# Kernel tuning notes

Hardware: AMD Instinct MI355X
Metric: run time of the kernel (lower is better)

Reference implementation:

```python
import jax, jax.numpy as jnp
import numpy as np

N, C, T = 64, 512, 64
P = N * (N - 1) // 2  # 2016 pairs


def _maxpool2x2(h):
    p, c, H, W = h.shape
    return h.reshape(p, c, H // 2, 2, W // 2, 2).max(axis=(3, 5))


def setup_inputs() -> dict:
    key = jax.random.key(0)
    ks = jax.random.split(key, 16)
    s = lambda k, shape, fan: jax.random.normal(k, shape, jnp.float32) * (1.0 / np.sqrt(fan))
    return {
        "x": jax.random.normal(ks[0], (N, C, T), jnp.float32),
        "w_conv1d": s(ks[1], (256, 512), 512),  # Conv1d(512,256,k=1) weight squeezed
        "b_conv1d": jnp.zeros((256,), jnp.float32),
        "w_c1": s(ks[2], (32, 512), 512),       # Conv2d(512,32,1x1)
        "b_c1": jnp.zeros((32,), jnp.float32),
        "w_c2": s(ks[3], (8, 32), 32),          # Conv2d(32,8,1x1)
        "b_c2": jnp.zeros((8,), jnp.float32),
        "w_fc1": s(ks[4], (32, 64), 64),
        "b_fc1": jnp.zeros((32,), jnp.float32),
        "w_fc2": s(ks[5], (8, 32), 32),
        "b_fc2": jnp.zeros((8,), jnp.float32),
        "w_fc3": s(ks[6], (1, 8), 8),
        "b_fc3": jnp.zeros((1,), jnp.float32),
        "w_mlp": s(ks[7], (1, C * T), C * T),   # stand-in my_fc: Linear(512*T,1)
        "b_mlp": jnp.zeros((1,), jnp.float32),
    }


def reference(x, w_conv1d, b_conv1d, w_c1, b_c1, w_c2, b_c2,
              w_fc1, b_fc1, w_fc2, b_fc2, w_fc3, b_fc3, w_mlp, b_mlp):
    # per-sample score head (my_fc stand-in)
    score = jax.nn.sigmoid(x.reshape(N, -1) @ w_mlp.T + b_mlp)  # [N,1]
    # shared conv1d over all samples at once (original does it per-pair)
    f = jnp.einsum("nct,oc->not", x, w_conv1d) + b_conv1d[None, :, None]  # [N,256,T]
    ii, jj = jnp.triu_indices(N, k=1)  # P pairs, same order as the nested loop
    # pairwise correlation matrix: einsum('abd,acd->abc')
    M = jnp.einsum("pct,pdt->pcd", f[ii], f[jj])  # [P,256,256]
    M = M.reshape(P, 512, 32, 4)
    h = jnp.einsum("pchw,oc->pohw", M, w_c1) + b_c1[None, :, None, None]
    h = _maxpool2x2(h)  # [P,32,16,2]
    h = jnp.einsum("pchw,oc->pohw", h, w_c2) + b_c2[None, :, None, None]
    h = _maxpool2x2(h)  # [P,8,8,1]
    v = h.reshape(P, 64)
    v = jax.nn.relu(v @ w_fc1.T + b_fc1)
    v = jax.nn.relu(v @ w_fc2.T + b_fc2)
    group_score = jax.nn.sigmoid(v @ w_fc3.T + b_fc3).reshape(-1)  # [P]
    return score, group_score
```

## Files before the change

### kernel.cpp

```cpp
#include <hip/hip_runtime.h>
#include <hip/hip_bf16.h>
#include <math.h>


typedef __attribute__((ext_vector_type(8))) short short8;
typedef __attribute__((ext_vector_type(4))) float f32x4;

__device__ __forceinline__ unsigned short f2bf(float f) {
    __hip_bfloat16 h = __float2bfloat16(f);
    return *reinterpret_cast<unsigned short*>(&h);
}

__global__ __launch_bounds__(256) void k_wa_part(
    const float* __restrict__ w_c1, const float* __restrict__ w_conv,
    float* __restrict__ Wpart)
{
    int b = blockIdx.x, q = blockIdx.y;
    int r = b >> 1;
    int cin = (b & 1) * 256 + threadIdx.x;
    int s = r >> 5, o = r & 31;
    const float* wrow = w_c1 + o * 512 + s;
    const float* wcp  = w_conv + cin;
    float acc = 0.f;
    #pragma unroll 8
    for (int c = q * 64; c < q * 64 + 64; ++c)
        acc += wrow[2 * c] * wcp[c * 512];
    Wpart[(q * 64 + r) * 512 + cin] = acc;
}

__global__ __launch_bounds__(256) void k_wprep(
    const float* __restrict__ w_conv1d, const float* __restrict__ Wpart,
    const float* __restrict__ b_conv1d, const float* __restrict__ w_c1,
    unsigned short* __restrict__ Wb, float* __restrict__ Gb)
{
    int idx = blockIdx.x * 256 + threadIdx.x;
    int m = idx >> 7, c4 = (idx & 127) * 4;
    float4 v;
    if (m < 256) {
        v = *reinterpret_cast<const float4*>(w_conv1d + m * 512 + c4);
    } else {
        const float* p0 = Wpart + (m - 256) * 512 + c4;
        float4 a = *reinterpret_cast<const float4*>(p0);
        float4 b = *reinterpret_cast<const float4*>(p0 + 32768);
        float4 c = *reinterpret_cast<const float4*>(p0 + 65536);
        float4 d = *reinterpret_cast<const float4*>(p0 + 98304);
        v.x = a.x + b.x + c.x + d.x;
        v.y = a.y + b.y + c.y + d.y;
        v.z = a.z + b.z + c.z + d.z;
        v.w = a.w + b.w + c.w + d.w;
    }
    ushort4 u;
    u.x = f2bf(v.x); u.y = f2bf(v.y); u.z = f2bf(v.z); u.w = f2bf(v.w);
    *reinterpret_cast<ushort4*>(Wb + m * 512 + c4) = u;

    if (blockIdx.x == 0) {
        __shared__ float abred[256];
        Gb[threadIdx.x] = b_conv1d[threadIdx.x];
        int r = threadIdx.x & 63, q = threadIdx.x >> 6;
        int s = r >> 5, o = r & 31;
        const float* wr2 = w_c1 + o * 512 + s;
        float a = 0.f;
        #pragma unroll 8
        for (int c = q * 64; c < q * 64 + 64; ++c)
            a += wr2[2 * c] * b_conv1d[c];
        abred[threadIdx.x] = a;
        __syncthreads();
        if (threadIdx.x < 64)
            Gb[256 + threadIdx.x] = abred[threadIdx.x] + abred[threadIdx.x + 64]
                                  + abred[threadIdx.x + 128] + abred[threadIdx.x + 192];
    }
}

__global__ __launch_bounds__(256) void k_xprep(
    const float* __restrict__ x, unsigned short* __restrict__ xxT)
{
    __shared__ float tile[64][65];
    int n = blockIdx.x, c0 = blockIdx.y * 64;
    int tid = threadIdx.x;
    int cl = tid >> 4, t4 = (tid & 15) * 4;
    const float* xp = x + n * 32768 + c0 * 64;
    #pragma unroll
    for (int p = 0; p < 4; ++p) {
        int c = cl + p * 16;
        float4 v = *reinterpret_cast<const float4*>(xp + c * 64 + t4);
        tile[t4 + 0][c] = v.x; tile[t4 + 1][c] = v.y;
        tile[t4 + 2][c] = v.z; tile[t4 + 3][c] = v.w;
    }
    __syncthreads();
    int tl = tid >> 4, cl4 = (tid & 15) * 4;
    #pragma unroll
    for (int p = 0; p < 4; ++p) {
        int t = tl + p * 16;
        ushort4 u;
        u.x = f2bf(tile[t][cl4 + 0]);
        u.y = f2bf(tile[t][cl4 + 1]);
        u.z = f2bf(tile[t][cl4 + 2]);
        u.w = f2bf(tile[t][cl4 + 3]);
        *reinterpret_cast<ushort4*>(xxT + n * 32768 + t * 512 + c0 + cl4) = u;
    }
}

__global__ __launch_bounds__(256) void k_fgemm(
    const unsigned short* __restrict__ Wb, const unsigned short* __restrict__ xxT,
    const float* __restrict__ Gb, unsigned short* __restrict__ FTTb,
    unsigned short* __restrict__ ALb)
{
    int n = blockIdx.x, mg = blockIdx.y, nt = blockIdx.z;
    int tid = threadIdx.x, l = tid & 63, w = tid >> 6;
    int m0 = mg * 64 + w * 16;
    int t0 = nt * 16;
    int r15 = l & 15, kg = l >> 4;
    const unsigned short* ap = Wb + (m0 + r15) * 512 + kg * 8;
    const unsigned short* bp = xxT + n * 32768 + (t0 + r15) * 512 + kg * 8;
    f32x4 acc = {0.f, 0.f, 0.f, 0.f};
    #pragma unroll
    for (int ks = 0; ks < 16; ++ks) {
        short8 a = *reinterpret_cast<const short8*>(ap + ks * 32);
        short8 b = *reinterpret_cast<const short8*>(bp + ks * 32);
        acc = __builtin_amdgcn_mfma_f32_16x16x32_bf16(a, b, acc, 0, 0, 0);
    }
    int t = t0 + r15;
    int mrow = m0 + kg * 4;
    float4 gb = *reinterpret_cast<const float4*>(Gb + mrow);
    float gbv[4] = {gb.x, gb.y, gb.z, gb.w};
    if (m0 < 256) {
        #pragma unroll
        for (int r = 0; r < 4; ++r) {
            int m = mrow + r;
            int e = m & 127, s = m >> 7, kp = s * 64 + t;
            int off = (((e << 8) + (kp << 1)) ^ ((e & 7) << 4)) >> 1;
            FTTb[n * 16384 + off] = f2bf(acc[r] + gbv[r]);
        }
    } else {
        #pragma unroll
        for (int r = 0; r < 4; ++r) {
            int m = mrow + r;
            int rr = m - 256, o = rr & 31, sA = rr >> 5, kp = sA * 64 + t;
            int off = (((o << 8) + (kp << 1)) ^ ((o & 7) << 4)) >> 1;
            ALb[n * 4096 + off] = f2bf(acc[r] + gbv[r]);
        }
    }
}

__global__ __launch_bounds__(256) void k_score_part(
    const float* __restrict__ x, const float* __restrict__ wm,
    float* __restrict__ part)
{
    int n = blockIdx.x, c4 = blockIdx.y;
    const float4* x4 = reinterpret_cast<const float4*>(x + n * 32768) + c4 * 2048;
    const float4* w4 = reinterpret_cast<const float4*>(wm) + c4 * 2048;
    float acc = 0.f;
    for (int u = threadIdx.x; u < 2048; u += 256) {
        float4 a = x4[u], w = w4[u];
        acc += a.x * w.x + a.y * w.y + a.z * w.z + a.w * w.w;
    }
    for (int off = 32; off; off >>= 1) acc += __shfl_down(acc, off, 64);
    __shared__ float red[4];
    if ((threadIdx.x & 63) == 0) red[threadIdx.x >> 6] = acc;
    __syncthreads();
    if (threadIdx.x == 0)
        part[n * 4 + c4] = red[0] + red[1] + red[2] + red[3];
}

__global__ __launch_bounds__(256) void k_pairs(
    const char* __restrict__ FTTb, const char* __restrict__ ALb,
    const float* __restrict__ b_c1, const float* __restrict__ w_c2,
    const float* __restrict__ b_c2, const float* __restrict__ w_fc1,
    const float* __restrict__ b_fc1, const float* __restrict__ w_fc2,
    const float* __restrict__ b_fc2, const float* __restrict__ w_fc3,
    const float* __restrict__ b_fc3, const float* __restrict__ part,
    const float* __restrict__ bm, float* __restrict__ out)
{
    __shared__ uint4 smq[2560];
    char* sm = (char*)smq;
    int p = blockIdx.x;
    int i = 0, rem = p;
    while (rem >= 63 - i) { rem -= 63 - i; ++i; }
    int j = i + 1 + rem;
    int tid = threadIdx.x;

    if (p == 0 && tid >= 128 && tid < 192) {
        int n = tid - 128;
        float s = part[n * 4] + part[n * 4 + 1] + part[n * 4 + 2]
                + part[n * 4 + 3] + bm[0];
        out[n] = 1.f / (1.f + expf(-s));
    }

    {
        const uint4* sA = reinterpret_cast<const uint4*>(ALb + (size_t)i * 8192);
        uint4* dA = reinterpret_cast<uint4*>(sm);
        #pragma unroll
        for (int u = 0; u < 2; ++u) dA[tid + 256 * u] = sA[tid + 256 * u];
        const uint4* sB = reinterpret_cast<const uint4*>(FTTb + (size_t)j * 32768);
        uint4* dB = reinterpret_cast<uint4*>(sm + 8192);
        #pragma unroll
        for (int u = 0; u < 8; ++u) dB[tid + 256 * u] = sB[tid + 256 * u];
    }
    __syncthreads();

    int l = tid & 63, wid = tid >> 6;
    int col = l & 15;
    int lk16 = (l >> 4) << 4;
    int xr = (col & 7) << 4;
    int oa0 = col, oa1 = col + 16;
    int e0 = wid * 32 + col, e1 = e0 + 16;

    f32x4 acc00 = {0.f,0.f,0.f,0.f}, acc01 = {0.f,0.f,0.f,0.f};
    f32x4 acc10 = {0.f,0.f,0.f,0.f}, acc11 = {0.f,0.f,0.f,0.f};
    #pragma unroll
    for (int ks = 0; ks < 4; ++ks) {
        int kb = ks * 64 + lk16;
        short8 a0 = *reinterpret_cast<const short8*>(sm + (((oa0 << 8) + kb) ^ xr));
        short8 a1 = *reinterpret_cast<const short8*>(sm + (((oa1 << 8) + kb) ^ xr));
        short8 b0 = *reinterpret_cast<const short8*>(sm + 8192 + (((e0 << 8) + kb) ^ xr));
        short8 b1 = *reinterpret_cast<const short8*>(sm + 8192 + (((e1 << 8) + kb) ^ xr));
        acc00 = __builtin_amdgcn_mfma_f32_16x16x32_bf16(a0, b0, acc00, 0, 0, 0);
        acc01 = __builtin_amdgcn_mfma_f32_16x16x32_bf16(a0, b1, acc01, 0, 0, 0);
        acc10 = __builtin_amdgcn_mfma_f32_16x16x32_bf16(a1, b0, acc10, 0, 0, 0);
        acc11 = __builtin_amdgcn_mfma_f32_16x16x32_bf16(a1, b1, acc11, 0, 0, 0);
    }
    __syncthreads();

    float* H = (float*)sm;
    int rowbase = (l >> 4) * 4;
    #pragma unroll
    for (int r4 = 0; r4 < 4; ++r4) {
        int o0 = rowbase + r4, o1 = o0 + 16;
        float bb0 = b_c1[o0], bb1 = b_c1[o1];
        H[o0 * 128 + e0] = acc00[r4] + bb0;
        H[o0 * 128 + e1] = acc01[r4] + bb0;
        H[o1 * 128 + e0] = acc10[r4] + bb1;
        H[o1 * 128 + e1] = acc11[r4] + bb1;
    }
    __syncthreads();

    float* PL = (float*)(sm + 16384);
    for (int idx = tid; idx < 1024; idx += 256) {
        int o = idx >> 5, h2 = (idx >> 1) & 15, w2 = idx & 1;
        const float* hp = H + o * 128 + h2 * 8 + w2 * 2;
        PL[o * 32 + h2 * 2 + w2] =
            fmaxf(fmaxf(hp[0], hp[1]), fmaxf(hp[4], hp[5]));
    }
    __syncthreads();

    float* C2 = (float*)(sm + 20480);
    {
        int o2 = tid >> 5, pos = tid & 31;
        float a2 = b_c2[o2];
        #pragma unroll 8
        for (int o = 0; o < 32; ++o) a2 += w_c2[o2 * 32 + o] * PL[o * 32 + pos];
        C2[o2 * 32 + pos] = a2;
    }
    __syncthreads();

    float* V = (float*)(sm + 21504);
    if (tid < 64) {
        int o2 = tid >> 3, h3 = tid & 7;
        const float* cp = C2 + o2 * 32 + h3 * 4;
        V[tid] = fmaxf(fmaxf(cp[0], cp[1]), fmaxf(cp[2], cp[3]));
    }
    __syncthreads();

    float* R1 = (float*)(sm + 21760);
    if (tid < 32) {
        float a = b_fc1[tid];
        const float* wr = w_fc1 + tid * 64;
        #pragma unroll 8
        for (int u = 0; u < 64; ++u) a += wr[u] * V[u];
        R1[tid] = fmaxf(a, 0.f);
    }
    __syncthreads();

    float* R2 = (float*)(sm + 21888);
    if (tid < 8) {
        float a = b_fc2[tid];
        #pragma unroll 8
        for (int u = 0; u < 32; ++u) a += w_fc2[tid * 32 + u] * R1[u];
        R2[tid] = fmaxf(a, 0.f);
    }
    __syncthreads();

    if (tid == 0) {
        float a = b_fc3[0];
        #pragma unroll
        for (int u = 0; u < 8; ++u) a += w_fc3[u] * R2[u];
        out[64 + p] = 1.f / (1.f + expf(-a));
    }
}

extern "C" void kernel_launch(void* const* d_in, const int* in_sizes, int n_in,
                              void* d_out, int out_size, void* d_ws, size_t ws_size,
                              hipStream_t stream) {
    const float* x        = (const float*)d_in[0];
    const float* w_conv1d = (const float*)d_in[1];
    const float* b_conv1d = (const float*)d_in[2];
    const float* w_c1     = (const float*)d_in[3];
    const float* b_c1     = (const float*)d_in[4];
    const float* w_c2     = (const float*)d_in[5];
    const float* b_c2     = (const float*)d_in[6];
    const float* w_fc1    = (const float*)d_in[7];
    const float* b_fc1    = (const float*)d_in[8];
    const float* w_fc2    = (const float*)d_in[9];
    const float* b_fc2    = (const float*)d_in[10];
    const float* w_fc3    = (const float*)d_in[11];
    const float* b_fc3    = (const float*)d_in[12];
    const float* w_mlp    = (const float*)d_in[13];
    const float* b_mlp    = (const float*)d_in[14];
    float* out = (float*)d_out;

    char* base = (char*)d_ws;
    unsigned short* xxT   = (unsigned short*)(base);
    unsigned short* FTTb  = (unsigned short*)(base + 4194304);
    unsigned short* ALb   = (unsigned short*)(base + 6291456);
    unsigned short* Wb    = (unsigned short*)(base + 6815744);
    float*          Wpart = (float*)(base + 7143424);
    float*          Gb    = (float*)(base + 7667712);
    float*          part  = (float*)(base + 7669760);

    hipLaunchKernelGGL(k_wa_part, dim3(128, 4), dim3(256), 0, stream,
                       w_c1, w_conv1d, Wpart);
    hipLaunchKernelGGL(k_wprep, dim3(160), dim3(256), 0, stream,
                       w_conv1d, Wpart, b_conv1d, w_c1, Wb, Gb);
    hipLaunchKernelGGL(k_xprep, dim3(64, 8), dim3(256), 0, stream, x, xxT);
    hipLaunchKernelGGL(k_score_part, dim3(64, 4), dim3(256), 0, stream,
                       x, w_mlp, part);
    hipLaunchKernelGGL(k_fgemm, dim3(64, 5, 4), dim3(256), 0, stream,
                       Wb, xxT, Gb, FTTb, ALb);
    hipLaunchKernelGGL(k_pairs, dim3(2016), dim3(256), 0, stream,
                       (const char*)FTTb, (const char*)ALb,
                       b_c1, w_c2, b_c2, w_fc1, b_fc1,
                       w_fc2, b_fc2, w_fc3, b_fc3, part, b_mlp, out);
}
```

Before: 141.3 us.

## Fuse all six kernels into one cooperative persistent kernel with grid syncs

Replaces the six separate launches with a single cooperative kernel of 512 persistent blocks. The stages are separated by grid-wide barriers, and each stage loops over its original work items. This removes the per-launch overhead and the gaps between kernels. In exchange it adds three grid.sync barriers, caps parallelism in the pairs stage at 512 resident blocks, and mixes the work item types of the first stage into one loop.

Measured after the change: 466.9 us. 230% more time.

```diff
diff --git a/kernel.cpp b/kernel.cpp
--- a/kernel.cpp
+++ b/kernel.cpp
@@ -1,6 +1,9 @@
 #include <hip/hip_runtime.h>
 #include <hip/hip_bf16.h>
+#include <hip/hip_cooperative_groups.h>
 #include <math.h>
+
+namespace cg = cooperative_groups;
 
 
 typedef __attribute__((ext_vector_type(8))) short short8;
@@ -11,280 +14,281 @@
     return *reinterpret_cast<unsigned short*>(&h);
 }
 
-__global__ __launch_bounds__(256) void k_wa_part(
-    const float* __restrict__ w_c1, const float* __restrict__ w_conv,
-    float* __restrict__ Wpart)
-{
-    int b = blockIdx.x, q = blockIdx.y;
-    int r = b >> 1;
-    int cin = (b & 1) * 256 + threadIdx.x;
-    int s = r >> 5, o = r & 31;
-    const float* wrow = w_c1 + o * 512 + s;
-    const float* wcp  = w_conv + cin;
-    float acc = 0.f;
-    #pragma unroll 8
-    for (int c = q * 64; c < q * 64 + 64; ++c)
-        acc += wrow[2 * c] * wcp[c * 512];
-    Wpart[(q * 64 + r) * 512 + cin] = acc;
-}
-
-__global__ __launch_bounds__(256) void k_wprep(
-    const float* __restrict__ w_conv1d, const float* __restrict__ Wpart,
+__global__ __launch_bounds__(256, 2) void k_mega(
+    const float* __restrict__ x, const float* __restrict__ w_conv1d,
     const float* __restrict__ b_conv1d, const float* __restrict__ w_c1,
-    unsigned short* __restrict__ Wb, float* __restrict__ Gb)
-{
-    int idx = blockIdx.x * 256 + threadIdx.x;
-    int m = idx >> 7, c4 = (idx & 127) * 4;
-    float4 v;
-    if (m < 256) {
-        v = *reinterpret_cast<const float4*>(w_conv1d + m * 512 + c4);
-    } else {
-        const float* p0 = Wpart + (m - 256) * 512 + c4;
-        float4 a = *reinterpret_cast<const float4*>(p0);
-        float4 b = *reinterpret_cast<const float4*>(p0 + 32768);
-        float4 c = *reinterpret_cast<const float4*>(p0 + 65536);
-        float4 d = *reinterpret_cast<const float4*>(p0 + 98304);
-        v.x = a.x + b.x + c.x + d.x;
-        v.y = a.y + b.y + c.y + d.y;
-        v.z = a.z + b.z + c.z + d.z;
-        v.w = a.w + b.w + c.w + d.w;
-    }
-    ushort4 u;
-    u.x = f2bf(v.x); u.y = f2bf(v.y); u.z = f2bf(v.z); u.w = f2bf(v.w);
-    *reinterpret_cast<ushort4*>(Wb + m * 512 + c4) = u;
-
-    if (blockIdx.x == 0) {
-        __shared__ float abred[256];
-        Gb[threadIdx.x] = b_conv1d[threadIdx.x];
-        int r = threadIdx.x & 63, q = threadIdx.x >> 6;
-        int s = r >> 5, o = r & 31;
-        const float* wr2 = w_c1 + o * 512 + s;
-        float a = 0.f;
-        #pragma unroll 8
-        for (int c = q * 64; c < q * 64 + 64; ++c)
-            a += wr2[2 * c] * b_conv1d[c];
-        abred[threadIdx.x] = a;
-        __syncthreads();
-        if (threadIdx.x < 64)
-            Gb[256 + threadIdx.x] = abred[threadIdx.x] + abred[threadIdx.x + 64]
-                                  + abred[threadIdx.x + 128] + abred[threadIdx.x + 192];
-    }
-}
-
-__global__ __launch_bounds__(256) void k_xprep(
-    const float* __restrict__ x, unsigned short* __restrict__ xxT)
-{
-    __shared__ float tile[64][65];
-    int n = blockIdx.x, c0 = blockIdx.y * 64;
-    int tid = threadIdx.x;
-    int cl = tid >> 4, t4 = (tid & 15) * 4;
-    const float* xp = x + n * 32768 + c0 * 64;
-    #pragma unroll
-    for (int p = 0; p < 4; ++p) {
-        int c = cl + p * 16;
-        float4 v = *reinterpret_cast<const float4*>(xp + c * 64 + t4);
-        tile[t4 + 0][c] = v.x; tile[t4 + 1][c] = v.y;
-        tile[t4 + 2][c] = v.z; tile[t4 + 3][c] = v.w;
-    }
-    __syncthreads();
-    int tl = tid >> 4, cl4 = (tid & 15) * 4;
-    #pragma unroll
-    for (int p = 0; p < 4; ++p) {
-        int t = tl + p * 16;
-        ushort4 u;
-        u.x = f2bf(tile[t][cl4 + 0]);
-        u.y = f2bf(tile[t][cl4 + 1]);
-        u.z = f2bf(tile[t][cl4 + 2]);
-        u.w = f2bf(tile[t][cl4 + 3]);
-        *reinterpret_cast<ushort4*>(xxT + n * 32768 + t * 512 + c0 + cl4) = u;
-    }
-}
-
-__global__ __launch_bounds__(256) void k_fgemm(
-    const unsigned short* __restrict__ Wb, const unsigned short* __restrict__ xxT,
-    const float* __restrict__ Gb, unsigned short* __restrict__ FTTb,
-    unsigned short* __restrict__ ALb)
-{
-    int n = blockIdx.x, mg = blockIdx.y, nt = blockIdx.z;
-    int tid = threadIdx.x, l = tid & 63, w = tid >> 6;
-    int m0 = mg * 64 + w * 16;
-    int t0 = nt * 16;
-    int r15 = l & 15, kg = l >> 4;
-    const unsigned short* ap = Wb + (m0 + r15) * 512 + kg * 8;
-    const unsigned short* bp = xxT + n * 32768 + (t0 + r15) * 512 + kg * 8;
-    f32x4 acc = {0.f, 0.f, 0.f, 0.f};
-    #pragma unroll
-    for (int ks = 0; ks < 16; ++ks) {
-        short8 a = *reinterpret_cast<const short8*>(ap + ks * 32);
-        short8 b = *reinterpret_cast<const short8*>(bp + ks * 32);
-        acc = __builtin_amdgcn_mfma_f32_16x16x32_bf16(a, b, acc, 0, 0, 0);
-    }
-    int t = t0 + r15;
-    int mrow = m0 + kg * 4;
-    float4 gb = *reinterpret_cast<const float4*>(Gb + mrow);
-    float gbv[4] = {gb.x, gb.y, gb.z, gb.w};
-    if (m0 < 256) {
-        #pragma unroll
-        for (int r = 0; r < 4; ++r) {
-            int m = mrow + r;
-            int e = m & 127, s = m >> 7, kp = s * 64 + t;
-            int off = (((e << 8) + (kp << 1)) ^ ((e & 7) << 4)) >> 1;
-            FTTb[n * 16384 + off] = f2bf(acc[r] + gbv[r]);
-        }
-    } else {
-        #pragma unroll
-        for (int r = 0; r < 4; ++r) {
-            int m = mrow + r;
-            int rr = m - 256, o = rr & 31, sA = rr >> 5, kp = sA * 64 + t;
-            int off = (((o << 8) + (kp << 1)) ^ ((o & 7) << 4)) >> 1;
-            ALb[n * 4096 + off] = f2bf(acc[r] + gbv[r]);
-        }
-    }
-}
-
-__global__ __launch_bounds__(256) void k_score_part(
-    const float* __restrict__ x, const float* __restrict__ wm,
-    float* __restrict__ part)
-{
-    int n = blockIdx.x, c4 = blockIdx.y;
-    const float4* x4 = reinterpret_cast<const float4*>(x + n * 32768) + c4 * 2048;
-    const float4* w4 = reinterpret_cast<const float4*>(wm) + c4 * 2048;
-    float acc = 0.f;
-    for (int u = threadIdx.x; u < 2048; u += 256) {
-        float4 a = x4[u], w = w4[u];
-        acc += a.x * w.x + a.y * w.y + a.z * w.z + a.w * w.w;
-    }
-    for (int off = 32; off; off >>= 1) acc += __shfl_down(acc, off, 64);
-    __shared__ float red[4];
-    if ((threadIdx.x & 63) == 0) red[threadIdx.x >> 6] = acc;
-    __syncthreads();
-    if (threadIdx.x == 0)
-        part[n * 4 + c4] = red[0] + red[1] + red[2] + red[3];
-}
-
-__global__ __launch_bounds__(256) void k_pairs(
-    const char* __restrict__ FTTb, const char* __restrict__ ALb,
     const float* __restrict__ b_c1, const float* __restrict__ w_c2,
     const float* __restrict__ b_c2, const float* __restrict__ w_fc1,
     const float* __restrict__ b_fc1, const float* __restrict__ w_fc2,
     const float* __restrict__ b_fc2, const float* __restrict__ w_fc3,
-    const float* __restrict__ b_fc3, const float* __restrict__ part,
-    const float* __restrict__ bm, float* __restrict__ out)
+    const float* __restrict__ b_fc3, const float* __restrict__ w_mlp,
+    const float* __restrict__ b_mlp,
+    unsigned short* __restrict__ xxT, unsigned short* __restrict__ FTTb,
+    unsigned short* __restrict__ ALb, unsigned short* __restrict__ Wb,
+    float* __restrict__ Wpart, float* __restrict__ Gb,
+    float* __restrict__ part, float* __restrict__ out)
 {
     __shared__ uint4 smq[2560];
     char* sm = (char*)smq;
-    int p = blockIdx.x;
-    int i = 0, rem = p;
-    while (rem >= 63 - i) { rem -= 63 - i; ++i; }
-    int j = i + 1 + rem;
-    int tid = threadIdx.x;
-
-    if (p == 0 && tid >= 128 && tid < 192) {
-        int n = tid - 128;
-        float s = part[n * 4] + part[n * 4 + 1] + part[n * 4 + 2]
-                + part[n * 4 + 3] + bm[0];
-        out[n] = 1.f / (1.f + expf(-s));
+    cg::grid_group grid = cg::this_grid();
+    int bid = blockIdx.x, tid = threadIdx.x;
+
+    for (int u = bid; u < 1280; u += 512) {
+        __syncthreads();
+        if (u < 512) {
+            int b = u & 127, q = u >> 7;
+            int r = b >> 1;
+            int cin = (b & 1) * 256 + tid;
+            int s = r >> 5, o = r & 31;
+            const float* wrow = w_c1 + o * 512 + s;
+            const float* wcp  = w_conv1d + cin;
+            float acc = 0.f;
+            #pragma unroll 8
+            for (int c = q * 64; c < q * 64 + 64; ++c)
+                acc += wrow[2 * c] * wcp[c * 512];
+            Wpart[(q * 64 + r) * 512 + cin] = acc;
+        } else if (u < 1024) {
+            int v = u - 512;
+            int n = v >> 3, c0 = (v & 7) * 64;
+            float* tile = (float*)sm;
+            int cl = tid >> 4, t4 = (tid & 15) * 4;
+            const float* xp = x + n * 32768 + c0 * 64;
+            #pragma unroll
+            for (int pp = 0; pp < 4; ++pp) {
+                int c = cl + pp * 16;
+                float4 vv = *reinterpret_cast<const float4*>(xp + c * 64 + t4);
+                tile[(t4 + 0) * 65 + c] = vv.x; tile[(t4 + 1) * 65 + c] = vv.y;
+                tile[(t4 + 2) * 65 + c] = vv.z; tile[(t4 + 3) * 65 + c] = vv.w;
+            }
+            __syncthreads();
+            int tl = tid >> 4, cl4 = (tid & 15) * 4;
+            #pragma unroll
+            for (int pp = 0; pp < 4; ++pp) {
+                int t = tl + pp * 16;
+                ushort4 uu;
+                uu.x = f2bf(tile[t * 65 + cl4 + 0]);
+                uu.y = f2bf(tile[t * 65 + cl4 + 1]);
+                uu.z = f2bf(tile[t * 65 + cl4 + 2]);
+                uu.w = f2bf(tile[t * 65 + cl4 + 3]);
+                *reinterpret_cast<ushort4*>(xxT + n * 32768 + t * 512 + c0 + cl4) = uu;
+            }
+        } else {
+            int v = u - 1024;
+            int n = v >> 2, c4 = v & 3;
+            const float4* x4 = reinterpret_cast<const float4*>(x + n * 32768) + c4 * 2048;
+            const float4* w4 = reinterpret_cast<const float4*>(w_mlp) + c4 * 2048;
+            float acc = 0.f;
+            #pragma unroll
+            for (int uu = tid, it = 0; it < 8; uu += 256, ++it) {
+                float4 a = x4[uu], w = w4[uu];
+                acc += a.x * w.x + a.y * w.y + a.z * w.z + a.w * w.w;
+            }
+            for (int off = 32; off; off >>= 1) acc += __shfl_down(acc, off, 64);
+            float* red = (float*)sm;
+            if ((tid & 63) == 0) red[tid >> 6] = acc;
+            __syncthreads();
+            if (tid == 0)
+                part[n * 4 + c4] = red[0] + red[1] + red[2] + red[3];
+        }
     }
-
-    {
-        const uint4* sA = reinterpret_cast<const uint4*>(ALb + (size_t)i * 8192);
-        uint4* dA = reinterpret_cast<uint4*>(sm);
+    __threadfence();
+    grid.sync();
+
+    if (bid < 160) {
+        int idx = bid * 256 + tid;
+        int m = idx >> 7, c4 = (idx & 127) * 4;
+        float4 v;
+        if (m < 256) {
+            v = *reinterpret_cast<const float4*>(w_conv1d + m * 512 + c4);
+        } else {
+            const float* p0 = Wpart + (m - 256) * 512 + c4;
+            float4 a = *reinterpret_cast<const float4*>(p0);
+            float4 b = *reinterpret_cast<const float4*>(p0 + 32768);
+            float4 c = *reinterpret_cast<const float4*>(p0 + 65536);
+            float4 d = *reinterpret_cast<const float4*>(p0 + 98304);
+            v.x = a.x + b.x + c.x + d.x;
+            v.y = a.y + b.y + c.y + d.y;
+            v.z = a.z + b.z + c.z + d.z;
+            v.w = a.w + b.w + c.w + d.w;
+        }
+        ushort4 uu;
+        uu.x = f2bf(v.x); uu.y = f2bf(v.y); uu.z = f2bf(v.z); uu.w = f2bf(v.w);
+        *reinterpret_cast<ushort4*>(Wb + m * 512 + c4) = uu;
+
+        if (bid == 0) {
+            float* abred = (float*)sm;
+            Gb[tid] = b_conv1d[tid];
+            int r = tid & 63, q = tid >> 6;
+            int s = r >> 5, o = r & 31;
+            const float* wr2 = w_c1 + o * 512 + s;
+            float a = 0.f;
+            #pragma unroll 8
+            for (int c = q * 64; c < q * 64 + 64; ++c)
+                a += wr2[2 * c] * b_conv1d[c];
+            abred[tid] = a;
+            __syncthreads();
+            if (tid < 64)
+                Gb[256 + tid] = abred[tid] + abred[tid + 64]
+                              + abred[tid + 128] + abred[tid + 192];
+        }
+    }
+    __threadfence();
+    grid.sync();
+
+    for (int u = bid; u < 1280; u += 512) {
+        int n = u / 20, rem = u - n * 20;
+        int mg = rem >> 2, nt = rem & 3;
+        int l = tid & 63, w = tid >> 6;
+        int m0 = mg * 64 + w * 16;
+        int t0 = nt * 16;
+        int r15 = l & 15, kg = l >> 4;
+        const unsigned short* ap = Wb + (m0 + r15) * 512 + kg * 8;
+        const unsigned short* bp = xxT + n * 32768 + (t0 + r15) * 512 + kg * 8;
+        f32x4 acc = {0.f, 0.f, 0.f, 0.f};
         #pragma unroll
-        for (int u = 0; u < 2; ++u) dA[tid + 256 * u] = sA[tid + 256 * u];
-        const uint4* sB = reinterpret_cast<const uint4*>(FTTb + (size_t)j * 32768);
-        uint4* dB = reinterpret_cast<uint4*>(sm + 8192);
+        for (int ks = 0; ks < 16; ++ks) {
+            short8 a = *reinterpret_cast<const short8*>(ap + ks * 32);
+            short8 b = *reinterpret_cast<const short8*>(bp + ks * 32);
+            acc = __builtin_amdgcn_mfma_f32_16x16x32_bf16(a, b, acc, 0, 0, 0);
+        }
+        int t = t0 + r15;
+        int mrow = m0 + kg * 4;
+        float4 gb = *reinterpret_cast<const float4*>(Gb + mrow);
+        float gbv[4] = {gb.x, gb.y, gb.z, gb.w};
+        if (m0 < 256) {
+            #pragma unroll
+            for (int r = 0; r < 4; ++r) {
+                int m = mrow + r;
+                int e = m & 127, s = m >> 7, kp = s * 64 + t;
+                int off = (((e << 8) + (kp << 1)) ^ ((e & 7) << 4)) >> 1;
+                FTTb[n * 16384 + off] = f2bf(acc[r] + gbv[r]);
+            }
+        } else {
+            #pragma unroll
+            for (int r = 0; r < 4; ++r) {
+                int m = mrow + r;
+                int rr = m - 256, o = rr & 31, sA = rr >> 5, kp = sA * 64 + t;
+                int off = (((o << 8) + (kp << 1)) ^ ((o & 7) << 4)) >> 1;
+                ALb[n * 4096 + off] = f2bf(acc[r] + gbv[r]);
+            }
+        }
+    }
+    __threadfence();
+    grid.sync();
+
+    for (int p = bid; p < 2016; p += 512) {
+        __syncthreads();
+        int i = 0, rem = p;
+        while (rem >= 63 - i) { rem -= 63 - i; ++i; }
+        int j = i + 1 + rem;
+
+        if (p == 0 && tid >= 128 && tid < 192) {
+            int n = tid - 128;
+            float s = part[n * 4] + part[n * 4 + 1] + part[n * 4 + 2]
+                    + part[n * 4 + 3] + b_mlp[0];
+            out[n] = 1.f / (1.f + expf(-s));
+        }
+
+        {
+            const uint4* sA = reinterpret_cast<const uint4*>((const char*)ALb + (size_t)i * 8192);
+            uint4* dA = reinterpret_cast<uint4*>(sm);
+            #pragma unroll
+            for (int u = 0; u < 2; ++u) dA[tid + 256 * u] = sA[tid + 256 * u];
+            const uint4* sB = reinterpret_cast<const uint4*>((const char*)FTTb + (size_t)j * 32768);
+            uint4* dB = reinterpret_cast<uint4*>(sm + 8192);
+            #pragma unroll
+            for (int u = 0; u < 8; ++u) dB[tid + 256 * u] = sB[tid + 256 * u];
+        }
+        __syncthreads();
+
+        int l = tid & 63, wid = tid >> 6;
+        int col = l & 15;
+        int lk16 = (l >> 4) << 4;
+        int xr = (col & 7) << 4;
+        int oa0 = col, oa1 = col + 16;
+        int e0 = wid * 32 + col, e1 = e0 + 16;
+
+        f32x4 acc00 = {0.f,0.f,0.f,0.f}, acc01 = {0.f,0.f,0.f,0.f};
+        f32x4 acc10 = {0.f,0.f,0.f,0.f}, acc11 = {0.f,0.f,0.f,0.f};
         #pragma unroll
-        for (int u = 0; u < 8; ++u) dB[tid + 256 * u] = sB[tid + 256 * u];
-    }
-    __syncthreads();
-
-    int l = tid & 63, wid = tid >> 6;
-    int col = l & 15;
-    int lk16 = (l >> 4) << 4;
-    int xr = (col & 7) << 4;
-    int oa0 = col, oa1 = col + 16;
-    int e0 = wid * 32 + col, e1 = e0 + 16;
-
-    f32x4 acc00 = {0.f,0.f,0.f,0.f}, acc01 = {0.f,0.f,0.f,0.f};
-    f32x4 acc10 = {0.f,0.f,0.f,0.f}, acc11 = {0.f,0.f,0.f,0.f};
-    #pragma unroll
-    for (int ks = 0; ks < 4; ++ks) {
-        int kb = ks * 64 + lk16;
-        short8 a0 = *reinterpret_cast<const short8*>(sm + (((oa0 << 8) + kb) ^ xr));
-        short8 a1 = *reinterpret_cast<const short8*>(sm + (((oa1 << 8) + kb) ^ xr));
-        short8 b0 = *reinterpret_cast<const short8*>(sm + 8192 + (((e0 << 8) + kb) ^ xr));
-        short8 b1 = *reinterpret_cast<const short8*>(sm + 8192 + (((e1 << 8) + kb) ^ xr));
-        acc00 = __builtin_amdgcn_mfma_f32_16x16x32_bf16(a0, b0, acc00, 0, 0, 0);
-        acc01 = __builtin_amdgcn_mfma_f32_16x16x32_bf16(a0, b1, acc01, 0, 0, 0);
-        acc10 = __builtin_amdgcn_mfma_f32_16x16x32_bf16(a1, b0, acc10, 0, 0, 0);
-        acc11 = __builtin_amdgcn_mfma_f32_16x16x32_bf16(a1, b1, acc11, 0, 0, 0);
-    }
-    __syncthreads();
-
-    float* H = (float*)sm;
-    int rowbase = (l >> 4) * 4;
-    #pragma unroll
-    for (int r4 = 0; r4 < 4; ++r4) {
-        int o0 = rowbase + r4, o1 = o0 + 16;
-        float bb0 = b_c1[o0], bb1 = b_c1[o1];
-        H[o0 * 128 + e0] = acc00[r4] + bb0;
-        H[o0 * 128 + e1] = acc01[r4] + bb0;
-        H[o1 * 128 + e0] = acc10[r4] + bb1;
-        H[o1 * 128 + e1] = acc11[r4] + bb1;
-    }
-    __syncthreads();
-
-    float* PL = (float*)(sm + 16384);
-    for (int idx = tid; idx < 1024; idx += 256) {
-        int o = idx >> 5, h2 = (idx >> 1) & 15, w2 = idx & 1;
-        const float* hp = H + o * 128 + h2 * 8 + w2 * 2;
-        PL[o * 32 + h2 * 2 + w2] =
-            fmaxf(fmaxf(hp[0], hp[1]), fmaxf(hp[4], hp[5]));
-    }
-    __syncthreads();
-
-    float* C2 = (float*)(sm + 20480);
-    {
-        int o2 = tid >> 5, pos = tid & 31;
-        float a2 = b_c2[o2];
-        #pragma unroll 8
-        for (int o = 0; o < 32; ++o) a2 += w_c2[o2 * 32 + o] * PL[o * 32 + pos];
-        C2[o2 * 32 + pos] = a2;
-    }
-    __syncthreads();
-
-    float* V = (float*)(sm + 21504);
-    if (tid < 64) {
-        int o2 = tid >> 3, h3 = tid & 7;
-        const float* cp = C2 + o2 * 32 + h3 * 4;
-        V[tid] = fmaxf(fmaxf(cp[0], cp[1]), fmaxf(cp[2], cp[3]));
-    }
-    __syncthreads();
-
-    float* R1 = (float*)(sm + 21760);
-    if (tid < 32) {
-        float a = b_fc1[tid];
-        const float* wr = w_fc1 + tid * 64;
-        #pragma unroll 8
-        for (int u = 0; u < 64; ++u) a += wr[u] * V[u];
-        R1[tid] = fmaxf(a, 0.f);
-    }
-    __syncthreads();
-
-    float* R2 = (float*)(sm + 21888);
-    if (tid < 8) {
-        float a = b_fc2[tid];
-        #pragma unroll 8
-        for (int u = 0; u < 32; ++u) a += w_fc2[tid * 32 + u] * R1[u];
-        R2[tid] = fmaxf(a, 0.f);
-    }
-    __syncthreads();
-
-    if (tid == 0) {
-        float a = b_fc3[0];
+        for (int ks = 0; ks < 4; ++ks) {
+            int kb = ks * 64 + lk16;
+            short8 a0 = *reinterpret_cast<const short8*>(sm + (((oa0 << 8) + kb) ^ xr));
+            short8 a1 = *reinterpret_cast<const short8*>(sm + (((oa1 << 8) + kb) ^ xr));
+            short8 b0 = *reinterpret_cast<const short8*>(sm + 8192 + (((e0 << 8) + kb) ^ xr));
+            short8 b1 = *reinterpret_cast<const short8*>(sm + 8192 + (((e1 << 8) + kb) ^ xr));
+            acc00 = __builtin_amdgcn_mfma_f32_16x16x32_bf16(a0, b0, acc00, 0, 0, 0);
+            acc01 = __builtin_amdgcn_mfma_f32_16x16x32_bf16(a0, b1, acc01, 0, 0, 0);
+            acc10 = __builtin_amdgcn_mfma_f32_16x16x32_bf16(a1, b0, acc10, 0, 0, 0);
+            acc11 = __builtin_amdgcn_mfma_f32_16x16x32_bf16(a1, b1, acc11, 0, 0, 0);
+        }
+        __syncthreads();
+
+        float* H = (float*)sm;
+        int rowbase = (l >> 4) * 4;
         #pragma unroll
-        for (int u = 0; u < 8; ++u) a += w_fc3[u] * R2[u];
-        out[64 + p] = 1.f / (1.f + expf(-a));
+        for (int r4 = 0; r4 < 4; ++r4) {
+            int o0 = rowbase + r4, o1 = o0 + 16;
+            float bb0 = b_c1[o0], bb1 = b_c1[o1];
+            H[o0 * 128 + e0] = acc00[r4] + bb0;
+            H[o0 * 128 + e1] = acc01[r4] + bb0;
+            H[o1 * 128 + e0] = acc10[r4] + bb1;
+            H[o1 * 128 + e1] = acc11[r4] + bb1;
+        }
+        __syncthreads();
+
+        float* PL = (float*)(sm + 16384);
+        for (int idx = tid; idx < 1024; idx += 256) {
+            int o = idx >> 5, h2 = (idx >> 1) & 15, w2 = idx & 1;
+            const float* hp = H + o * 128 + h2 * 8 + w2 * 2;
+            PL[o * 32 + h2 * 2 + w2] =
+                fmaxf(fmaxf(hp[0], hp[1]), fmaxf(hp[4], hp[5]));
+        }
+        __syncthreads();
+
+        float* C2 = (float*)(sm + 20480);
+        {
+            int o2 = tid >> 5, pos = tid & 31;
+            float a2 = b_c2[o2];
+            #pragma unroll 8
+            for (int o = 0; o < 32; ++o) a2 += w_c2[o2 * 32 + o] * PL[o * 32 + pos];
+            C2[o2 * 32 + pos] = a2;
+        }
+        __syncthreads();
+
+        float* V = (float*)(sm + 21504);
+        if (tid < 64) {
+            int o2 = tid >> 3, h3 = tid & 7;
+            const float* cp = C2 + o2 * 32 + h3 * 4;
+            V[tid] = fmaxf(fmaxf(cp[0], cp[1]), fmaxf(cp[2], cp[3]));
+        }
+        __syncthreads();
+
+        float* R1 = (float*)(sm + 21760);
+        if (tid < 32) {
+            float a = b_fc1[tid];
+            const float* wr = w_fc1 + tid * 64;
+            #pragma unroll 8
+            for (int u = 0; u < 64; ++u) a += wr[u] * V[u];
+            R1[tid] = fmaxf(a, 0.f);
+        }
+        __syncthreads();
+
+        float* R2 = (float*)(sm + 21888);
+        if (tid < 8) {
+            float a = b_fc2[tid];
+            #pragma unroll 8
+            for (int u = 0; u < 32; ++u) a += w_fc2[tid * 32 + u] * R1[u];
+            R2[tid] = fmaxf(a, 0.f);
+        }
+        __syncthreads();
+
+        if (tid == 0) {
+            float a = b_fc3[0];
+            #pragma unroll
+            for (int u = 0; u < 8; ++u) a += w_fc3[u] * R2[u];
+            out[64 + p] = 1.f / (1.f + expf(-a));
+        }
     }
 }
 
@@ -317,17 +321,14 @@
     float*          Gb    = (float*)(base + 7667712);
     float*          part  = (float*)(base + 7669760);
 
-    hipLaunchKernelGGL(k_wa_part, dim3(128, 4), dim3(256), 0, stream,
-                       w_c1, w_conv1d, Wpart);
-    hipLaunchKernelGGL(k_wprep, dim3(160), dim3(256), 0, stream,
-                       w_conv1d, Wpart, b_conv1d, w_c1, Wb, Gb);
-    hipLaunchKernelGGL(k_xprep, dim3(64, 8), dim3(256), 0, stream, x, xxT);
-    hipLaunchKernelGGL(k_score_part, dim3(64, 4), dim3(256), 0, stream,
-                       x, w_mlp, part);
-    hipLaunchKernelGGL(k_fgemm, dim3(64, 5, 4), dim3(256), 0, stream,
-                       Wb, xxT, Gb, FTTb, ALb);
-    hipLaunchKernelGGL(k_pairs, dim3(2016), dim3(256), 0, stream,
-                       (const char*)FTTb, (const char*)ALb,
-                       b_c1, w_c2, b_c2, w_fc1, b_fc1,
-                       w_fc2, b_fc2, w_fc3, b_fc3, part, b_mlp, out);
+    void* args[] = {
+        (void*)&x, (void*)&w_conv1d, (void*)&b_conv1d, (void*)&w_c1,
+        (void*)&b_c1, (void*)&w_c2, (void*)&b_c2, (void*)&w_fc1,
+        (void*)&b_fc1, (void*)&w_fc2, (void*)&b_fc2, (void*)&w_fc3,
+        (void*)&b_fc3, (void*)&w_mlp, (void*)&b_mlp,
+        (void*)&xxT, (void*)&FTTb, (void*)&ALb, (void*)&Wb,
+        (void*)&Wpart, (void*)&Gb, (void*)&part, (void*)&out
+    };
+    hipLaunchCooperativeKernel((const void*)k_mega, dim3(512), dim3(256),
+                               args, 0, stream);
 }
```
